# Kernel tuning notes

Hardware: AMD Instinct MI355X
Metric: run time of the kernel (lower is better)

Reference implementation:

```python
import jax, jax.numpy as jnp
import numpy as np

B, N, D = 32, 2048, 1024


def setup_inputs() -> dict:
    key = jax.random.key(0)
    k1, k2, k3, k4, k5, k6 = jax.random.split(key, 6)
    encoded = jax.random.normal(k1, (B, N, D), dtype=jnp.float32)
    decoder_state = jax.random.normal(k2, (B, D), dtype=jnp.float32)
    mask = jax.random.randint(k3, (B, N), 0, 2, dtype=jnp.int32)
    scale = 1.0 / np.sqrt(D)
    W1 = jax.random.normal(k4, (D, D), dtype=jnp.float32) * scale  # applied as x @ W1
    W2 = jax.random.normal(k5, (D, D), dtype=jnp.float32) * scale
    vt = jax.random.normal(k6, (D,), dtype=jnp.float32) * scale
    return {"encoded": encoded, "decoder_state": decoder_state, "mask": mask,
            "W1": W1, "W2": W2, "vt": vt}


def reference(encoded, decoder_state, mask, W1, W2, vt):
    temperature = 1.0
    # process_encoded: W1(encoded)  [B, N, D]
    enc = jnp.einsum('bnd,de->bne', encoded, W1)
    # W2(decoder_state)  [B, D] -> broadcast-add over N
    dec = decoder_state @ W2
    # vt(tanh(.)).squeeze(2)  -> logits [B, N]
    u = jnp.einsum('bnd,d->bn', jnp.tanh(enc + dec[:, None, :]), vt)
    # masked log-softmax with temperature over dim=1
    logits = u / temperature + jnp.log(mask.astype(u.dtype) + 1e-45)
    return jax.nn.log_softmax(logits, axis=1)
```

## Files before the change

kernel.cpp:

```cpp
#include <hip/hip_runtime.h>

typedef _Float16 half8 __attribute__((ext_vector_type(8)));
typedef __fp16   pk2   __attribute__((ext_vector_type(2)));
typedef float    f32x4 __attribute__((ext_vector_type(4)));

#define GLOBAL_AS __attribute__((address_space(1)))
#define LDS_AS    __attribute__((address_space(3)))

static constexpr int Bb = 32;
static constexpr int Nn = 2048;
static constexpr int Dd = 1024;
static constexpr int M  = Bb * Nn;


__global__ void prep_w1(const float* __restrict__ W1, _Float16* __restrict__ W1TT) {
    int g = blockIdx.x * 256 + threadIdx.x;
    int chunk = g >> 10;
    int u = g & 1023;
    int q = u >> 7, sc = u & 127;
    int cl = sc ^ (2 * (q & 3));
    int et = chunk >> 5, t = (chunk >> 1) & 15, h = chunk & 1;
    int e  = et * 256 + h * 128 + cl;
    int k0 = t * 64 + q * 8;
    half8 hh;
#pragma unroll
    for (int j = 0; j < 8; ++j)
        hh[j] = (_Float16)W1[(size_t)(k0 + j) * Dd + e];
    *(half8*)(W1TT + (size_t)g * 8) = hh;
}

__global__ void prep_enc(const float* __restrict__ A, _Float16* __restrict__ A_p) {
    __shared__ _Float16 T[128 * 64];
    const int c = blockIdx.x;
    const int tid = threadIdx.x;
    const int mtile = c >> 5, t = (c >> 1) & 15, h = c & 1;
    const int r = tid >> 1, kh = tid & 1;
    const float* src = A + (size_t)(mtile * 256 + h * 128 + r) * Dd + t * 64 + kh * 32;
    const int rx = r & 7;
#pragma unroll
    for (int i = 0; i < 4; ++i) {
        f32x4 a  = *(const f32x4*)(src + i * 8);
        f32x4 b2 = *(const f32x4*)(src + i * 8 + 4);
        half8 hh; pk2 p;
        p = __builtin_amdgcn_cvt_pkrtz(a.x, a.y);   hh[0] = p[0]; hh[1] = p[1];
        p = __builtin_amdgcn_cvt_pkrtz(a.z, a.w);   hh[2] = p[0]; hh[3] = p[1];
        p = __builtin_amdgcn_cvt_pkrtz(b2.x, b2.y); hh[4] = p[0]; hh[5] = p[1];
        p = __builtin_amdgcn_cvt_pkrtz(b2.z, b2.w); hh[6] = p[0]; hh[7] = p[1];
        *(half8*)(T + r * 64 + (((kh * 4 + i) ^ rx) * 8)) = hh;
    }
    __syncthreads();
    const size_t cb = (size_t)c * 8192;
#pragma unroll
    for (int i = 0; i < 4; ++i) {
        int u = i * 256 + tid;
        int q = u >> 7, sr = u & 127;
        int lr = sr ^ (2 * (q & 3));
        half8 hh = *(const half8*)(T + lr * 64 + ((q ^ (lr & 7)) * 8));
        *(half8*)(A_p + cb + (size_t)u * 8) = hh;
    }
}

__global__ void dec_kernel(const float* __restrict__ ds, const float* __restrict__ W2,
                           float* __restrict__ dec) {
    __shared__ float part[4][64];
    int b = blockIdx.x, ech = blockIdx.y;
    int tid = threadIdx.x;
    int e = ech * 64 + (tid & 63);
    int dc = tid >> 6;
    float acc = 0.f;
#pragma unroll 4
    for (int d = dc * 256; d < dc * 256 + 256; ++d)
        acc += ds[b * Dd + d] * W2[(size_t)d * Dd + e];
    part[dc][tid & 63] = acc;
    __syncthreads();
    if (tid < 64)
        dec[b * Dd + e] = part[0][tid] + part[1][tid] + part[2][tid] + part[3][tid];
}

__global__ __launch_bounds__(512) void gemm8(
    const _Float16* __restrict__ A_p, const _Float16* __restrict__ W1TT,
    const float* __restrict__ dec, const float* __restrict__ vt,
    float* __restrict__ u_part)
{
    extern __shared__ _Float16 lds[];

    const int g  = blockIdx.x;
    const int wg = (g & 7) * 128 + (g >> 3);
    const int et    = wg & 3;
    const int mtile = wg >> 2;

    const int tid  = threadIdx.x;
    const int lane = tid & 63, wid = tid >> 6;
    const int wr = wid >> 2, wc = wid & 3;
    const int qq = lane >> 4, l15 = lane & 15;
    const int l15s = l15 ^ (2 * qq);
    const int rA = wr * 16 + l15s;
    const int rB = wc * 16 + l15s;

    f32x4 acc[8][4] = {};

    const int b = mtile >> 3;
    float vtv[4], dcv[4];
#pragma unroll
    for (int nf = 0; nf < 4; ++nf) {
        int e = et * 256 + (nf >> 1) * 128 + (nf & 1) * 64 + wc * 16 + l15;
        vtv[nf] = vt[e];
        dcv[nf] = dec[b * Dd + e];
    }
    asm volatile("s_waitcnt vmcnt(0)" ::: "memory");

    const size_t abase = (size_t)mtile * 32 * 8192;
    const size_t bbase = (size_t)et * 32 * 8192;
    const int uoff = tid * 8;

    auto stA = [&](int t2, int h) {
        const _Float16* gp = A_p + abase + ((size_t)(t2 * 2 + h) << 13) + uoff;
        _Float16* lp = lds + ((((t2 & 1) * 2 + h) << 13) + (wid << 9));
        __builtin_amdgcn_global_load_lds((const GLOBAL_AS void*)gp,
                                         (LDS_AS void*)lp, 16, 0, 0);
        __builtin_amdgcn_global_load_lds((const GLOBAL_AS void*)(gp + 4096),
                                         (LDS_AS void*)(lp + 4096), 16, 0, 0);
    };
    auto stB = [&](int t2, int h) {
        const _Float16* gp = W1TT + bbase + ((size_t)(t2 * 2 + h) << 13) + uoff;
        _Float16* lp = lds + (32768 + (((t2 & 1) * 2 + h) << 13) + (wid << 9));
        __builtin_amdgcn_global_load_lds((const GLOBAL_AS void*)gp,
                                         (LDS_AS void*)lp, 16, 0, 0);
        __builtin_amdgcn_global_load_lds((const GLOBAL_AS void*)(gp + 4096),
                                         (LDS_AS void*)(lp + 4096), 16, 0, 0);
    };

    stA(0, 0); stB(0, 0); stB(0, 1); stA(0, 1); stA(1, 0); stB(1, 0); stB(1, 1);
    asm volatile("s_waitcnt vmcnt(10)" ::: "memory");
    asm volatile("s_barrier" ::: "memory");

    half8 af[4][2], bf0[2][2], bf1[2][2];

#pragma unroll 1
    for (int t = 0; t < 16; ++t) {
        const int Ab0 = (t & 1) * 16384;
        const int Ab1 = Ab0 + 8192;
        const int Bb0 = 32768 + Ab0;
        const int Bb1 = Bb0 + 8192;

#pragma unroll
        for (int ks = 0; ks < 2; ++ks) {
            const int qb = ((ks * 4 + qq) * 128) * 8;
#pragma unroll
            for (int m = 0; m < 4; ++m)
                af[m][ks] = *(const half8*)&lds[Ab0 + qb + (m * 32 + rA) * 8];
#pragma unroll
            for (int j = 0; j < 2; ++j)
                bf0[j][ks] = *(const half8*)&lds[Bb0 + qb + (j * 64 + rB) * 8];
        }
        if (t < 15) stA(t + 1, 1);
        if (t < 15) asm volatile("s_waitcnt vmcnt(10)" ::: "memory");
        else        asm volatile("s_waitcnt vmcnt(2)"  ::: "memory");
        asm volatile("s_barrier" ::: "memory");
        asm volatile("s_waitcnt lgkmcnt(0)" ::: "memory");
        __builtin_amdgcn_s_setprio(1);
#pragma unroll
        for (int m = 0; m < 4; ++m)
#pragma unroll
            for (int j = 0; j < 2; ++j) {
                acc[m][j] = __builtin_amdgcn_mfma_f32_16x16x32_f16(af[m][0], bf0[j][0], acc[m][j], 0, 0, 0);
                acc[m][j] = __builtin_amdgcn_mfma_f32_16x16x32_f16(af[m][1], bf0[j][1], acc[m][j], 0, 0, 0);
            }
        __builtin_amdgcn_s_setprio(0);
        asm volatile("s_barrier" ::: "memory");

#pragma unroll
        for (int ks = 0; ks < 2; ++ks) {
            const int qb = ((ks * 4 + qq) * 128) * 8;
#pragma unroll
            for (int j = 0; j < 2; ++j)
                bf1[j][ks] = *(const half8*)&lds[Bb1 + qb + (j * 64 + rB) * 8];
        }
        if (t < 14) stA(t + 2, 0);
        if (t < 14)       asm volatile("s_waitcnt vmcnt(10)" ::: "memory");
        else if (t == 14) asm volatile("s_waitcnt vmcnt(8)"  ::: "memory");
        else              asm volatile("s_waitcnt vmcnt(0)"  ::: "memory");
        asm volatile("s_barrier" ::: "memory");
        asm volatile("s_waitcnt lgkmcnt(0)" ::: "memory");
        __builtin_amdgcn_s_setprio(1);
#pragma unroll
        for (int m = 0; m < 4; ++m)
#pragma unroll
            for (int j = 0; j < 2; ++j) {
                acc[m][2 + j] = __builtin_amdgcn_mfma_f32_16x16x32_f16(af[m][0], bf1[j][0], acc[m][2 + j], 0, 0, 0);
                acc[m][2 + j] = __builtin_amdgcn_mfma_f32_16x16x32_f16(af[m][1], bf1[j][1], acc[m][2 + j], 0, 0, 0);
            }
        __builtin_amdgcn_s_setprio(0);
        asm volatile("s_barrier" ::: "memory");

#pragma unroll
        for (int ks = 0; ks < 2; ++ks) {
            const int qb = ((ks * 4 + qq) * 128) * 8;
#pragma unroll
            for (int m = 0; m < 4; ++m)
                af[m][ks] = *(const half8*)&lds[Ab1 + qb + (m * 32 + rA) * 8];
        }
        if (t < 14) stB(t + 2, 0);
        asm volatile("s_barrier" ::: "memory");
        asm volatile("s_waitcnt lgkmcnt(0)" ::: "memory");
        __builtin_amdgcn_s_setprio(1);
#pragma unroll
        for (int m = 0; m < 4; ++m)
#pragma unroll
            for (int j = 0; j < 2; ++j) {
                acc[4 + m][j] = __builtin_amdgcn_mfma_f32_16x16x32_f16(af[m][0], bf0[j][0], acc[4 + m][j], 0, 0, 0);
                acc[4 + m][j] = __builtin_amdgcn_mfma_f32_16x16x32_f16(af[m][1], bf0[j][1], acc[4 + m][j], 0, 0, 0);
            }
        __builtin_amdgcn_s_setprio(0);
        asm volatile("s_barrier" ::: "memory");

        if (t < 14) stB(t + 2, 1);
        if (t < 14)       asm volatile("s_waitcnt vmcnt(10)" ::: "memory");
        else if (t == 14) asm volatile("s_waitcnt vmcnt(4)"  ::: "memory");
        asm volatile("s_barrier" ::: "memory");
        __builtin_amdgcn_s_setprio(1);
#pragma unroll
        for (int m = 0; m < 4; ++m)
#pragma unroll
            for (int j = 0; j < 2; ++j) {
                acc[4 + m][2 + j] = __builtin_amdgcn_mfma_f32_16x16x32_f16(af[m][0], bf1[j][0], acc[4 + m][2 + j], 0, 0, 0);
                acc[4 + m][2 + j] = __builtin_amdgcn_mfma_f32_16x16x32_f16(af[m][1], bf1[j][1], acc[4 + m][2 + j], 0, 0, 0);
            }
        __builtin_amdgcn_s_setprio(0);
        asm volatile("s_barrier" ::: "memory");
    }

    float* usum = (float*)lds;
#pragma unroll
    for (int hm = 0; hm < 8; ++hm) {
        const int h = hm >> 2, m = hm & 3;
#pragma unroll
        for (int r = 0; r < 4; ++r) {
            float s = 0.f;
#pragma unroll
            for (int nf = 0; nf < 4; ++nf) {
                float x  = acc[hm][nf][r] + dcv[nf];
                float ex = __expf(2.f * x);
                s += (1.f - 2.f * __builtin_amdgcn_rcpf(ex + 1.f)) * vtv[nf];
            }
#pragma unroll
            for (int off = 1; off < 16; off <<= 1) s += __shfl_xor(s, off, 16);
            if (l15 == 0)
                usum[wc * 256 + h * 128 + m * 32 + wr * 16 + qq * 4 + r] = s;
        }
    }
    __syncthreads();
    if (tid < 256) {
        float v = usum[tid] + usum[256 + tid] + usum[512 + tid] + usum[768 + tid];
        u_part[(size_t)et * M + (size_t)mtile * 256 + tid] = v;
    }
}

__global__ void softmax_k(const float* __restrict__ up, const int* __restrict__ mask,
                          float* __restrict__ out) {
    __shared__ float red[8];
    int b = blockIdx.x, tid = threadIdx.x;
    float l[8];
#pragma unroll
    for (int i = 0; i < 8; ++i) {
        int n = i * 256 + tid;
        float s = up[(size_t)b * Nn + n];
#pragma unroll
        for (int et = 1; et < 4; ++et) s += up[(size_t)et * M + (size_t)b * Nn + n];
        l[i] = s + (mask[b * Nn + n] ? 0.f : -103.278931f);
    }
    float m = l[0];
#pragma unroll
    for (int i = 1; i < 8; ++i) m = fmaxf(m, l[i]);
#pragma unroll
    for (int o = 32; o >= 1; o >>= 1) m = fmaxf(m, __shfl_xor(m, o, 64));
    if ((tid & 63) == 0) red[tid >> 6] = m;
    __syncthreads();
    m = fmaxf(fmaxf(red[0], red[1]), fmaxf(red[2], red[3]));
    float s = 0.f;
#pragma unroll
    for (int i = 0; i < 8; ++i) s += expf(l[i] - m);
#pragma unroll
    for (int o = 32; o >= 1; o >>= 1) s += __shfl_xor(s, o, 64);
    if ((tid & 63) == 0) red[4 + (tid >> 6)] = s;
    __syncthreads();
    float lse = m + logf(red[4] + red[5] + red[6] + red[7]);
#pragma unroll
    for (int i = 0; i < 8; ++i)
        out[(size_t)b * Nn + i * 256 + tid] = l[i] - lse;
}

extern "C" void kernel_launch(void* const* d_in, const int* in_sizes, int n_in,
                              void* d_out, int out_size, void* d_ws, size_t ws_size,
                              hipStream_t stream) {
    const float* encoded = (const float*)d_in[0];
    const float* dstate  = (const float*)d_in[1];
    const int*   mask    = (const int*)d_in[2];
    const float* W1      = (const float*)d_in[3];
    const float* W2      = (const float*)d_in[4];
    const float* vt      = (const float*)d_in[5];
    float* out = (float*)d_out;

    char* ws = (char*)d_ws;
    float*    u_part = (float*)ws;
    float*    dec    = (float*)(ws + (size_t)4 * M * 4);
    _Float16* W1TT   = (_Float16*)(ws + (size_t)4 * M * 4 + (size_t)Bb * Dd * 4);
    _Float16* A_p    = (_Float16*)(ws + (size_t)4 * M * 4 + (size_t)Bb * Dd * 4
                                   + (size_t)Dd * Dd * 2);

    static bool attr_done = false;
    if (!attr_done) {
        hipFuncSetAttribute(reinterpret_cast<const void*>(gemm8),
                            hipFuncAttributeMaxDynamicSharedMemorySize, 131072);
        attr_done = true;
    }

    prep_w1<<<512, 256, 0, stream>>>(W1, W1TT);
    dec_kernel<<<dim3(32, 16), 256, 0, stream>>>(dstate, W2, dec);
    prep_enc<<<8192, 256, 0, stream>>>(encoded, A_p);
    gemm8<<<1024, 512, 131072, stream>>>(A_p, W1TT, dec, vt, u_part);
    softmax_k<<<32, 256, 0, stream>>>(u_part, mask, out);
}
```

Baseline: 569.7 us.

## Restructure GEMM main loop into double-register ping-pong pipeline with partial waits

Rewrites the MFMA main loop to unroll two K-tiles per iteration, with two A and two B fragment register sets. LDS reads for the next quadrant are issued before the current MFMA block, and full lgkmcnt(0) waits are replaced by partial lgkmcnt counts, so LDS latency overlaps matrix math. The order of global-to-LDS loads is reshuffled, and the vt/dec loads move after the loop so the prologue no longer waits on them. This raises register pressure and relies on exact wait counts being right, so a miscount could cause races.

Measured after the change: 574.9 us. No clear change (+0.9%).

```diff
diff --git a/kernel.cpp b/kernel.cpp
--- a/kernel.cpp
+++ b/kernel.cpp
@@ -77,6 +77,29 @@
         dec[b * Dd + e] = part[0][tid] + part[1][tid] + part[2][tid] + part[3][tid];
 }
 
+#define BAR     asm volatile("s_barrier" ::: "memory")
+#define LGKM(n) asm volatile("s_waitcnt lgkmcnt(" #n ")" ::: "memory")
+#define VM(n)   asm volatile("s_waitcnt vmcnt(" #n ")" ::: "memory")
+
+#define RD_A(dst, base) do { _Pragma("unroll") \
+  for (int ks = 0; ks < 2; ++ks) { const int qb = ((ks * 4 + qq) * 128) * 8; \
+    _Pragma("unroll") for (int m2 = 0; m2 < 4; ++m2) \
+      dst[m2][ks] = *(const half8*)&lds[(base) + qb + (m2 * 32 + rA) * 8]; } } while (0)
+
+#define RD_B(dst, base) do { _Pragma("unroll") \
+  for (int ks = 0; ks < 2; ++ks) { const int qb = ((ks * 4 + qq) * 128) * 8; \
+    _Pragma("unroll") for (int j2 = 0; j2 < 2; ++j2) \
+      dst[j2][ks] = *(const half8*)&lds[(base) + qb + (j2 * 64 + rB) * 8]; } } while (0)
+
+#define MFMAQ(A_, B_, ro, co) do { __builtin_amdgcn_s_setprio(1); \
+  _Pragma("unroll") for (int m2 = 0; m2 < 4; ++m2) \
+  _Pragma("unroll") for (int j2 = 0; j2 < 2; ++j2) { \
+    acc[(ro) + m2][(co) + j2] = __builtin_amdgcn_mfma_f32_16x16x32_f16( \
+        A_[m2][0], B_[j2][0], acc[(ro) + m2][(co) + j2], 0, 0, 0); \
+    acc[(ro) + m2][(co) + j2] = __builtin_amdgcn_mfma_f32_16x16x32_f16( \
+        A_[m2][1], B_[j2][1], acc[(ro) + m2][(co) + j2], 0, 0, 0); } \
+  __builtin_amdgcn_s_setprio(0); } while (0)
+
 __global__ __launch_bounds__(512) void gemm8(
     const _Float16* __restrict__ A_p, const _Float16* __restrict__ W1TT,
     const float* __restrict__ dec, const float* __restrict__ vt,
@@ -98,16 +121,7 @@
     const int rB = wc * 16 + l15s;
 
     f32x4 acc[8][4] = {};
-
-    const int b = mtile >> 3;
-    float vtv[4], dcv[4];
-#pragma unroll
-    for (int nf = 0; nf < 4; ++nf) {
-        int e = et * 256 + (nf >> 1) * 128 + (nf & 1) * 64 + wc * 16 + l15;
-        vtv[nf] = vt[e];
-        dcv[nf] = dec[b * Dd + e];
-    }
-    asm volatile("s_waitcnt vmcnt(0)" ::: "memory");
+    half8 a0[4][2], a1[4][2], b0[2][2], b1[2][2];
 
     const size_t abase = (size_t)mtile * 32 * 8192;
     const size_t bbase = (size_t)et * 32 * 8192;
@@ -130,106 +144,79 @@
                                          (LDS_AS void*)(lp + 4096), 16, 0, 0);
     };
 
-    stA(0, 0); stB(0, 0); stB(0, 1); stA(0, 1); stA(1, 0); stB(1, 0); stB(1, 1);
-    asm volatile("s_waitcnt vmcnt(10)" ::: "memory");
-    asm volatile("s_barrier" ::: "memory");
-
-    half8 af[4][2], bf0[2][2], bf1[2][2];
+    stA(0, 0); stB(0, 1); stA(0, 1); stB(0, 0); stA(1, 0); stB(1, 1);
+    VM(4);
+    BAR;
+    RD_A(a0, 0);
+    RD_B(b0, 32768);
 
 #pragma unroll 1
-    for (int t = 0; t < 16; ++t) {
-        const int Ab0 = (t & 1) * 16384;
-        const int Ab1 = Ab0 + 8192;
-        const int Bb0 = 32768 + Ab0;
-        const int Bb1 = Bb0 + 8192;
-
-#pragma unroll
-        for (int ks = 0; ks < 2; ++ks) {
-            const int qb = ((ks * 4 + qq) * 128) * 8;
-#pragma unroll
-            for (int m = 0; m < 4; ++m)
-                af[m][ks] = *(const half8*)&lds[Ab0 + qb + (m * 32 + rA) * 8];
-#pragma unroll
-            for (int j = 0; j < 2; ++j)
-                bf0[j][ks] = *(const half8*)&lds[Bb0 + qb + (j * 64 + rB) * 8];
-        }
-        if (t < 15) stA(t + 1, 1);
-        if (t < 15) asm volatile("s_waitcnt vmcnt(10)" ::: "memory");
-        else        asm volatile("s_waitcnt vmcnt(2)"  ::: "memory");
-        asm volatile("s_barrier" ::: "memory");
-        asm volatile("s_waitcnt lgkmcnt(0)" ::: "memory");
-        __builtin_amdgcn_s_setprio(1);
-#pragma unroll
-        for (int m = 0; m < 4; ++m)
-#pragma unroll
-            for (int j = 0; j < 2; ++j) {
-                acc[m][j] = __builtin_amdgcn_mfma_f32_16x16x32_f16(af[m][0], bf0[j][0], acc[m][j], 0, 0, 0);
-                acc[m][j] = __builtin_amdgcn_mfma_f32_16x16x32_f16(af[m][1], bf0[j][1], acc[m][j], 0, 0, 0);
-            }
-        __builtin_amdgcn_s_setprio(0);
-        asm volatile("s_barrier" ::: "memory");
-
-#pragma unroll
-        for (int ks = 0; ks < 2; ++ks) {
-            const int qb = ((ks * 4 + qq) * 128) * 8;
-#pragma unroll
-            for (int j = 0; j < 2; ++j)
-                bf1[j][ks] = *(const half8*)&lds[Bb1 + qb + (j * 64 + rB) * 8];
-        }
-        if (t < 14) stA(t + 2, 0);
-        if (t < 14)       asm volatile("s_waitcnt vmcnt(10)" ::: "memory");
-        else if (t == 14) asm volatile("s_waitcnt vmcnt(8)"  ::: "memory");
-        else              asm volatile("s_waitcnt vmcnt(0)"  ::: "memory");
-        asm volatile("s_barrier" ::: "memory");
-        asm volatile("s_waitcnt lgkmcnt(0)" ::: "memory");
-        __builtin_amdgcn_s_setprio(1);
-#pragma unroll
-        for (int m = 0; m < 4; ++m)
-#pragma unroll
-            for (int j = 0; j < 2; ++j) {
-                acc[m][2 + j] = __builtin_amdgcn_mfma_f32_16x16x32_f16(af[m][0], bf1[j][0], acc[m][2 + j], 0, 0, 0);
-                acc[m][2 + j] = __builtin_amdgcn_mfma_f32_16x16x32_f16(af[m][1], bf1[j][1], acc[m][2 + j], 0, 0, 0);
-            }
-        __builtin_amdgcn_s_setprio(0);
-        asm volatile("s_barrier" ::: "memory");
-
-#pragma unroll
-        for (int ks = 0; ks < 2; ++ks) {
-            const int qb = ((ks * 4 + qq) * 128) * 8;
-#pragma unroll
-            for (int m = 0; m < 4; ++m)
-                af[m][ks] = *(const half8*)&lds[Ab1 + qb + (m * 32 + rA) * 8];
-        }
-        if (t < 14) stB(t + 2, 0);
-        asm volatile("s_barrier" ::: "memory");
-        asm volatile("s_waitcnt lgkmcnt(0)" ::: "memory");
-        __builtin_amdgcn_s_setprio(1);
-#pragma unroll
-        for (int m = 0; m < 4; ++m)
-#pragma unroll
-            for (int j = 0; j < 2; ++j) {
-                acc[4 + m][j] = __builtin_amdgcn_mfma_f32_16x16x32_f16(af[m][0], bf0[j][0], acc[4 + m][j], 0, 0, 0);
-                acc[4 + m][j] = __builtin_amdgcn_mfma_f32_16x16x32_f16(af[m][1], bf0[j][1], acc[4 + m][j], 0, 0, 0);
-            }
-        __builtin_amdgcn_s_setprio(0);
-        asm volatile("s_barrier" ::: "memory");
-
-        if (t < 14) stB(t + 2, 1);
-        if (t < 14)       asm volatile("s_waitcnt vmcnt(10)" ::: "memory");
-        else if (t == 14) asm volatile("s_waitcnt vmcnt(4)"  ::: "memory");
-        asm volatile("s_barrier" ::: "memory");
-        __builtin_amdgcn_s_setprio(1);
-#pragma unroll
-        for (int m = 0; m < 4; ++m)
-#pragma unroll
-            for (int j = 0; j < 2; ++j) {
-                acc[4 + m][2 + j] = __builtin_amdgcn_mfma_f32_16x16x32_f16(af[m][0], bf1[j][0], acc[4 + m][2 + j], 0, 0, 0);
-                acc[4 + m][2 + j] = __builtin_amdgcn_mfma_f32_16x16x32_f16(af[m][1], bf1[j][1], acc[4 + m][2 + j], 0, 0, 0);
-            }
-        __builtin_amdgcn_s_setprio(0);
-        asm volatile("s_barrier" ::: "memory");
-    }
-
+    for (int i = 0; i < 8; ++i) {
+        const int E = 2 * i, O = E + 1;
+        const bool nl = (i < 7);
+
+        RD_B(b1, 32768 + 8192);
+        stA(O, 1);
+        BAR; LGKM(4);
+        MFMAQ(a0, b0, 0, 0);
+        BAR;
+
+        RD_A(a1, 8192);
+        stB(O, 0);
+        BAR; LGKM(8);
+        MFMAQ(a0, b1, 0, 2);
+        VM(6);
+        BAR;
+
+        RD_A(a0, 16384);
+        if (nl) stA(E + 2, 0);
+        BAR; LGKM(8);
+        MFMAQ(a1, b1, 4, 2);
+        BAR;
+
+        if (nl) { stB(E + 2, 1); VM(4); }
+        else    { VM(0); }
+        BAR;
+        MFMAQ(a1, b0, 4, 0);
+        RD_B(b0, 32768 + 16384);
+        BAR;
+
+        RD_B(b1, 32768 + 16384 + 8192);
+        if (nl) stA(E + 2, 1);
+        BAR; LGKM(4);
+        MFMAQ(a0, b0, 0, 0);
+        BAR;
+
+        RD_A(a1, 16384 + 8192);
+        if (nl) stB(E + 2, 0);
+        BAR; LGKM(8);
+        MFMAQ(a0, b1, 0, 2);
+        VM(6);
+        BAR;
+
+        if (nl) { RD_A(a0, 0);
+                  stA(O + 2, 0); }
+        BAR;
+        if (nl) { LGKM(8); } else { LGKM(0); }
+        MFMAQ(a1, b1, 4, 2);
+        BAR;
+
+        if (nl) stB(O + 2, 1);
+        VM(4);
+        BAR;
+        MFMAQ(a1, b0, 4, 0);
+        if (nl) RD_B(b0, 32768);
+        BAR;
+    }
+
+    const int b = mtile >> 3;
+    float vtv[4], dcv[4];
+#pragma unroll
+    for (int nf = 0; nf < 4; ++nf) {
+        int e = et * 256 + (nf >> 1) * 128 + (nf & 1) * 64 + wc * 16 + l15;
+        vtv[nf] = vt[e];
+        dcv[nf] = dec[b * Dd + e];
+    }
     float* usum = (float*)lds;
 #pragma unroll
     for (int hm = 0; hm < 8; ++hm) {
```
